# Performance work log

Measured on AMD Instinct MI355X. Metric: run time of the kernel, lower is better.

Reference implementation:

```python
import jax, jax.numpy as jnp
import numpy as np

NEG_SLOPE = 0.01

def lrelu(x):
    return jax.nn.leaky_relu(x, NEG_SLOPE)

def lin(x, w, b):
    # torch Linear: x @ W.T + b, W shape (out, in)
    return x @ w.T + b

def meansum_pool(mask, x_local, *x_global):
    # masked sum + mean over points, concat with global/context vectors
    x_sum = (x_local * mask).sum(axis=1)                 # (b, d)
    x_mean = x_sum / mask.sum(axis=1)                    # (b, d) / (b, 1)
    return jnp.concatenate([x_mean, x_sum, *x_global], axis=1)


def setup_inputs() -> dict:
    key = jax.random.key(0)
    ks = jax.random.split(key, 16)
    B, N, DIN, DC, H, G, NB, DOUT = 16, 8192, 3, 16, 128, 10, 6, 3

    def w(k, shape, fan_in):
        return (jax.random.normal(k, shape, jnp.float32) / np.float32(np.sqrt(fan_in)))

    inp = {
        "x_local": jax.random.normal(ks[0], (B, N, DIN), jnp.float32),
        "context": jax.random.normal(ks[1], (B, DC), jnp.float32),
        "mask": (jax.random.uniform(ks[2], (B, N, 1)) < 0.9).astype(jnp.float32),
        # EPiC_Projection params (effective weight-normed weights)
        "proj_lw": w(ks[3], (H, DIN), DIN), "proj_lb": jnp.zeros((H,), jnp.float32),
        "proj_g0w": w(ks[4], (H, 2 * H + DC), 2 * H + DC), "proj_g0b": jnp.zeros((H,), jnp.float32),
        "proj_g1w": w(ks[5], (H, H), H), "proj_g1b": jnp.zeros((H,), jnp.float32),
        "proj_g2w": w(ks[6], (G, H), H), "proj_g2b": jnp.zeros((G,), jnp.float32),
        # stacked per-block EPiC_layer params
        "g1w": w(ks[7], (NB, H, 2 * H + G + DC), 2 * H + G + DC), "g1b": jnp.zeros((NB, H), jnp.float32),
        "g2w": w(ks[8], (NB, G, H), H), "g2b": jnp.zeros((NB, G), jnp.float32),
        "l1w": w(ks[9], (NB, H, H + G + DC), H + G + DC), "l1b": jnp.zeros((NB, H), jnp.float32),
        "l2w": w(ks[10], (NB, H, H), H), "l2b": jnp.zeros((NB, H), jnp.float32),
        # output head
        "outw": w(ks[11], (DOUT, H), H), "outb": jnp.zeros((DOUT,), jnp.float32),
    }
    return inp


def reference(x_local, context, mask,
              proj_lw, proj_lb, proj_g0w, proj_g0b, proj_g1w, proj_g1b, proj_g2w, proj_g2b,
              g1w, g1b, g2w, g2b, l1w, l1b, l2w, l2b, outw, outb):
    B, N, _ = x_local.shape
    # --- EPiC_Projection ---
    xl = lrelu(lin(x_local, proj_lw, proj_lb))           # (b, n, H)
    xg = meansum_pool(mask, xl, context)                 # (b, 2H + DC)
    xg = lrelu(lin(xg, proj_g0w, proj_g0b))
    xg = lrelu(lin(xg, proj_g1w, proj_g1b))
    xg = lrelu(lin(xg, proj_g2w, proj_g2b))              # (b, G)
    xl = xl * mask
    # --- EPiC layers (no skip: use_skip_connection=False -> +0) ---
    num_blocks = g1w.shape[0]
    for i in range(num_blocks):
        pooled = meansum_pool(mask, xl, xg, context)     # (b, 2H + G + DC)
        h_g = lrelu(lin(pooled, g1w[i], g1b[i]))
        xg = lrelu(lin(h_g, g2w[i], g2b[i]) + xg)        # residual global
        xg_b = jnp.broadcast_to(xg[:, None, :], (B, N, xg.shape[-1]))
        ctx_b = jnp.broadcast_to(context[:, None, :], (B, N, context.shape[-1]))
        cat = jnp.concatenate([xl, xg_b, ctx_b], axis=2)  # (b, n, H + G + DC)
        h_l = lrelu(lin(cat, l1w[i], l1b[i]))
        xl = lrelu(lin(h_l, l2w[i], l2b[i]) + xl) * mask  # residual local, masked
    h = lin(xl, outw, outb)                              # (b, n, 3)
    return h * mask
```

## Files before the change

### kernel.cpp

```cpp
#include <hip/hip_runtime.h>
#include <hip/hip_bf16.h>


typedef __attribute__((ext_vector_type(8))) short short8;
typedef __attribute__((ext_vector_type(4))) float f32x4;

#define B_ 16
#define N_ 8192
#define DC_ 16
#define H_ 128
#define G_ 10
#define NB_ 6
#define NEG_ 0.01f

__device__ __forceinline__ float lrelu(float x) { return x > 0.f ? x : NEG_ * x; }

__device__ __forceinline__ unsigned short f2bf(float x) {
  union { float f; unsigned u; } v; v.f = x;
  return (unsigned short)((v.u + 0x7fffu + ((v.u >> 16) & 1u)) >> 16);
}
__device__ __forceinline__ float bf2f(unsigned short u) {
  union { unsigned u; float f; } v; v.u = ((unsigned)u) << 16; return v.f;
}
__device__ __forceinline__ void split_bf(float x, unsigned short& h, unsigned short& l) {
  h = f2bf(x);
  l = f2bf(x - bf2f(h));
}

__device__ __forceinline__ f32x4 mfma16(short8 a, short8 b, f32x4 c) {
  return __builtin_amdgcn_mfma_f32_16x16x32_bf16(a, b, c, 0, 0, 0);
}

__device__ __forceinline__ void make_frags(f32x4 v0, f32x4 v1, short8& bh, short8& bl) {
  unsigned short h, l;
#pragma unroll
  for (int j = 0; j < 4; ++j) {
    split_bf(v0[j], h, l);
    bh[j] = (short)h; bl[j] = (short)l;
  }
#pragma unroll
  for (int j = 0; j < 4; ++j) {
    split_bf(v1[j], h, l);
    bh[4 + j] = (short)h; bl[4 + j] = (short)l;
  }
}

__device__ __forceinline__ void async_cp16(const void* g, void* l) {
  __builtin_amdgcn_global_load_lds(
      (const __attribute__((address_space(1))) void*)g,
      (__attribute__((address_space(3))) void*)l, 16, 0, 0);
}

__device__ __forceinline__ void agent_store(float* p, float v) {
  __hip_atomic_store(p, v, __ATOMIC_RELAXED, __HIP_MEMORY_SCOPE_AGENT);
}
__device__ __forceinline__ float agent_load(const float* p) {
  return __hip_atomic_load(p, __ATOMIC_RELAXED, __HIP_MEMORY_SCOPE_AGENT);
}

template <int NS>
__device__ void epic_global_tail(
    int b, int tid, const float* __restrict__ pP, float cnt,
    const float* __restrict__ xg_cur, float* __restrict__ xg_next,
    const float* __restrict__ context,
    const float* __restrict__ g1w_n, const float* __restrict__ g1b_n,
    const float* __restrict__ g2w_n, const float* __restrict__ g2b_n,
    const float* __restrict__ l1w_n, const float* __restrict__ l1b_n,
    float* __restrict__ gbias_out, float* shx) {
  {
    const int f = tid & 127, kh = tid >> 7;
    const float* pr = pP + ((size_t)b * NS + kh * (NS / 2)) * 128 + f;
    float s = 0.f;
#pragma unroll 8
    for (int w = 0; w < NS / 2; ++w) s += agent_load(pr + w * 128);
    shx[tid] = s;
  }
  __syncthreads();
  if (tid < 128) {
    float s = shx[tid] + shx[tid + 128];
    shx[384 + tid] = s;
    shx[256 + tid] = s / cnt;
  }
  if (tid < G_) shx[512 + tid] = xg_cur[tid];
  if (tid < DC_) shx[522 + tid] = context[b * DC_ + tid];
  __syncthreads();
  {
    const int f = tid & 127, kh = tid >> 7;
    const float* wr = g1w_n + (size_t)f * 282 + kh * 142;
    const float* vp = shx + 256 + kh * 142;
    const int n2 = kh ? 70 : 71;
    float a = 0.f;
#pragma unroll 8
    for (int j = 0; j < n2; ++j) {
      float2 w2 = *(const float2*)(wr + 2 * j);
      a += w2.x * vp[2 * j] + w2.y * vp[2 * j + 1];
    }
    __syncthreads();
    shx[tid] = a;
  }
  __syncthreads();
  if (tid < 128) shx[544 + tid] = lrelu(shx[tid] + shx[tid + 128] + g1b_n[tid]);
  __syncthreads();
  if (tid < G_) {
    const float* wr = g2w_n + tid * 128;
    float a = g2b_n[tid] + shx[512 + tid];
#pragma unroll 8
    for (int j = 0; j < 32; ++j) {
      float4 w4 = *(const float4*)(wr + 4 * j);
      a += w4.x * shx[544 + 4 * j] + w4.y * shx[544 + 4 * j + 1] +
           w4.z * shx[544 + 4 * j + 2] + w4.w * shx[544 + 4 * j + 3];
    }
    float v = lrelu(a);
    shx[672 + tid] = v;
    xg_next[tid] = v;
  }
  __syncthreads();
  if (tid < 128) {
    const float* wr = l1w_n + tid * 154;
    float a = l1b_n[tid];
#pragma unroll
    for (int j = 0; j < G_; ++j) a += wr[128 + j] * shx[672 + j];
#pragma unroll
    for (int j = 0; j < DC_; ++j) a += wr[138 + j] * shx[522 + j];
    gbias_out[tid] = a;
  }
}

__global__ __launch_bounds__(256) void prep_weights(
    const float* __restrict__ l1w, const float* __restrict__ l2w,
    unsigned short* __restrict__ w1h, unsigned short* __restrict__ w1l,
    unsigned short* __restrict__ w2h, unsigned short* __restrict__ w2l,
    unsigned int* __restrict__ counters) {
  int idx = blockIdx.x * 256 + threadIdx.x;
  const int total = NB_ * H_ * H_;
  if (idx < 112) counters[idx] = 0u;
  if (idx < total) {
    int i = idx / (H_ * H_), rem = idx % (H_ * H_);
    int F = rem / H_, k = rem % H_;
    int mt = F >> 4, r = F & 15, ks = k >> 5, c = k & 31;
    int off = i * 16384 + (mt * 4 + ks) * 512 + ((c >> 3) * 16 + r) * 8 + (c & 7);
    unsigned short h, l;
    split_bf(l1w[(i * H_ + F) * 154 + k], h, l);
    w1h[off] = h; w1l[off] = l;
    split_bf(l2w[(i * H_ + F) * H_ + k], h, l);
    w2h[off] = h; w2l[off] = l;
  }
}

__global__ __launch_bounds__(256, 2) void proj_local_kernel(
    const float* __restrict__ xloc, const float* __restrict__ maskp,
    const float* __restrict__ plw, const float* __restrict__ plb,
    float* __restrict__ xlf, float* __restrict__ pP,
    float* __restrict__ cntp, float* __restrict__ cnt_g,
    unsigned int* __restrict__ counters,
    const float* __restrict__ context,
    const float* __restrict__ g0w, const float* __restrict__ g0b,
    const float* __restrict__ g1pw, const float* __restrict__ g1pb,
    const float* __restrict__ g2pw, const float* __restrict__ g2pb,
    float* __restrict__ xg_g,
    const float* __restrict__ g1w0, const float* __restrict__ g1b0,
    const float* __restrict__ g2w0, const float* __restrict__ g2b0,
    const float* __restrict__ l1w0, const float* __restrict__ l1b0,
    float* __restrict__ gbias_g) {
  __shared__ float wq[H_][4];
  __shared__ float wsum[512];
  __shared__ float cw[4];
  __shared__ float shx[768];
  __shared__ int winflag;
  const int tid = threadIdx.x, bid = blockIdx.x;
  const int wv = tid >> 6, lane = tid & 63;
  const int q = lane >> 4, n16 = lane & 15;
  const int b = bid >> 6;
  if (tid < H_) {
    wq[tid][0] = plw[tid * 3 + 0];
    wq[tid][1] = plw[tid * 3 + 1];
    wq[tid][2] = plw[tid * 3 + 2];
    wq[tid][3] = plb[tid];
  }
  __syncthreads();
  const int t = bid * 4 + wv;
  const int p0 = t * 32;
  const int pa = p0 + n16, pb = p0 + 16 + n16;
  const float xa0 = xloc[pa * 3], xa1 = xloc[pa * 3 + 1], xa2 = xloc[pa * 3 + 2];
  const float xb0 = xloc[pb * 3], xb1 = xloc[pb * 3 + 1], xb2 = xloc[pb * 3 + 2];
  const float m0 = maskp[pa], m1 = maskp[pb];
  float* ga = xlf + (size_t)(2 * t) * 2048;
  float* gb = ga + 2048;
#pragma unroll
  for (int ms = 0; ms < 8; ++ms) {
    f32x4 v0, v1;
#pragma unroll
    for (int r = 0; r < 4; ++r) {
      const int F = ms * 16 + q * 4 + r;
      float4 w4 = *(const float4*)wq[F];
      v0[r] = lrelu(w4.x * xa0 + w4.y * xa1 + w4.z * xa2 + w4.w) * m0;
      v1[r] = lrelu(w4.x * xb0 + w4.y * xb1 + w4.z * xb2 + w4.w) * m1;
    }
    *(f32x4*)(ga + ms * 256 + (q * 16 + n16) * 4) = v0;
    *(f32x4*)(gb + ms * 256 + (q * 16 + n16) * 4) = v1;
    f32x4 s = v0 + v1;
#pragma unroll
    for (int r = 0; r < 4; ++r) {
      float sv = s[r];
      sv += __shfl_xor(sv, 1, 64);
      sv += __shfl_xor(sv, 2, 64);
      sv += __shfl_xor(sv, 4, 64);
      sv += __shfl_xor(sv, 8, 64);
      s[r] = sv;
    }
    if (n16 == 0) *(f32x4*)&wsum[wv * 128 + ms * 16 + q * 4] = s;
  }
  {
    float c = (q == 0) ? (m0 + m1) : 0.f;
    c += __shfl_xor(c, 1, 64);
    c += __shfl_xor(c, 2, 64);
    c += __shfl_xor(c, 4, 64);
    c += __shfl_xor(c, 8, 64);
    if (lane == 0) cw[wv] = c;
  }
  __syncthreads();
  if (tid < 128) {
    agent_store(&pP[(size_t)(2 * bid) * 128 + tid], wsum[tid] + wsum[128 + tid]);
    agent_store(&pP[(size_t)(2 * bid + 1) * 128 + tid], wsum[256 + tid] + wsum[384 + tid]);
  }
  if (tid == 0) agent_store(&cntp[bid], cw[0] + cw[1] + cw[2] + cw[3]);

  __syncthreads();
  if (tid == 0) winflag = (atomicAdd(&counters[b], 1u) == 63u) ? 1 : 0;
  __syncthreads();
  if (!winflag) return;
  if (tid < 64) shx[688 + tid] = agent_load(&cntp[b * 64 + tid]);
  __syncthreads();
  if (tid == 0) {
    float c = 0.f;
#pragma unroll
    for (int w = 0; w < 64; ++w) c += shx[688 + w];
    shx[752] = c;
    cnt_g[b] = c;
  }
  __syncthreads();
  const float cnt = shx[752];
  {
    const int f = tid & 127, kh = tid >> 7;
    const float* pr = pP + ((size_t)b * 128 + kh * 64) * 128 + f;
    float s = 0.f;
#pragma unroll 8
    for (int w = 0; w < 64; ++w) s += agent_load(pr + w * 128);
    shx[tid] = s;
  }
  __syncthreads();
  if (tid < 128) {
    float s = shx[tid] + shx[tid + 128];
    shx[384 + tid] = s;
    shx[256 + tid] = s / cnt;
  }
  if (tid < DC_) shx[512 + tid] = context[b * DC_ + tid];
  __syncthreads();
  {
    const int f = tid & 127, kh = tid >> 7;
    const float* wr = g0w + (size_t)f * 272 + kh * 136;
    const float* vp = shx + 256 + kh * 136;
    float a = 0.f;
#pragma unroll 8
    for (int j = 0; j < 34; ++j) {
      float4 w4 = *(const float4*)(wr + 4 * j);
      a += w4.x * vp[4 * j] + w4.y * vp[4 * j + 1] + w4.z * vp[4 * j + 2] + w4.w * vp[4 * j + 3];
    }
    __syncthreads();
    shx[tid] = a;
  }
  __syncthreads();
  if (tid < 128) shx[544 + tid] = lrelu(shx[tid] + shx[tid + 128] + g0b[tid]);
  __syncthreads();
  {
    const int f = tid & 127, kh = tid >> 7;
    const float* wr = g1pw + (size_t)f * 128 + kh * 64;
    const float* vp = shx + 544 + kh * 64;
    float a = 0.f;
#pragma unroll 8
    for (int j = 0; j < 16; ++j) {
      float4 w4 = *(const float4*)(wr + 4 * j);
      a += w4.x * vp[4 * j] + w4.y * vp[4 * j + 1] + w4.z * vp[4 * j + 2] + w4.w * vp[4 * j + 3];
    }
    __syncthreads();
    shx[tid] = a;
  }
  __syncthreads();
  if (tid < 128) shx[544 + tid] = lrelu(shx[tid] + shx[tid + 128] + g1pb[tid]);
  __syncthreads();
  if (tid < G_) {
    const float* wr = g2pw + tid * 128;
    float a = g2pb[tid];
#pragma unroll 8
    for (int j = 0; j < 32; ++j) {
      float4 w4 = *(const float4*)(wr + 4 * j);
      a += w4.x * shx[544 + 4 * j] + w4.y * shx[544 + 4 * j + 1] +
           w4.z * shx[544 + 4 * j + 2] + w4.w * shx[544 + 4 * j + 3];
    }
    xg_g[(0 * 16 + b) * 16 + tid] = lrelu(a);
  }
  __syncthreads();
  epic_global_tail<128>(b, tid, pP, cnt,
                        xg_g + (0 * 16 + b) * 16, xg_g + (1 * 16 + b) * 16, context,
                        g1w0, g1b0, g2w0, g2b0, l1w0, l1b0,
                        gbias_g + (size_t)(0 * 16 + b) * 128, shx);
}

template <bool LAST>
__global__ __launch_bounds__(256, 1) void epic_local_kernel(
    float* __restrict__ xlf, float* __restrict__ pP,
    const float* __restrict__ cnt_g, unsigned int* __restrict__ counters_blk,
    const float* __restrict__ gbias_in,
    const float* __restrict__ xg_tail_cur, float* __restrict__ xg_tail_next,
    float* __restrict__ gbias_tail_out,
    const float* __restrict__ context,
    const float* __restrict__ g1w_n, const float* __restrict__ g1b_n,
    const float* __restrict__ g2w_n, const float* __restrict__ g2b_n,
    const float* __restrict__ l1w_n, const float* __restrict__ l1b_n,
    const float* __restrict__ l2b,
    const unsigned short* __restrict__ w1h, const unsigned short* __restrict__ w1l,
    const unsigned short* __restrict__ w2h, const unsigned short* __restrict__ w2l,
    const float* __restrict__ maskp,
    const float* __restrict__ outw, const float* __restrict__ outb,
    float* __restrict__ outp) {
  __shared__ unsigned short wbuf[65536];
  __shared__ float tiles[4][576];
  __shared__ float shx[768];
  __shared__ float gbias_s[128];
  __shared__ float l2b_s[128];
  __shared__ float wsum[512];
  __shared__ float outw_s[392];
  __shared__ int winflag;
  const int tid = threadIdx.x, bid = blockIdx.x;
  const int b = bid >> 5;
  const int wv = tid >> 6, lane = tid & 63;
  const int q = lane >> 4, n16 = lane & 15;

  {
    const unsigned short* src = (wv == 0) ? w1h : (wv == 1) ? w1l : (wv == 2) ? w2h : w2l;
    const char* s8 = (const char*)src + lane * 16;
    char* d8 = (char*)&wbuf[wv * 16384];
#pragma unroll
    for (int j = 0; j < 32; ++j) async_cp16(s8 + j * 1024, d8 + j * 1024);
  }
  if (tid < 128) {
    gbias_s[tid] = gbias_in[b * 128 + tid];
    l2b_s[tid] = l2b[tid];
  }
  if (LAST) {
    for (int i = tid; i < 384; i += 256) outw_s[i] = outw[i];
    if (tid < 3) outw_s[384 + tid] = outb[tid];
  }

  const int g0i = bid * 16 + wv * 4;
  short8 xbh[4][4], xbl[4][4];
#pragma unroll
  for (int nt = 0; nt < 4; ++nt) {
    const float* base_nt = xlf + (size_t)(g0i + nt) * 2048;
#pragma unroll
    for (int ks = 0; ks < 4; ++ks) {
      const float* pb = base_nt + (2 * ks + (q >> 1)) * 256 + ((q & 1) * 32 + n16) * 4;
      f32x4 v0 = *(const f32x4*)pb;
      f32x4 v1 = *(const f32x4*)(pb + 64);
      make_frags(v0, v1, xbh[nt][ks], xbl[nt][ks]);
    }
  }
  __syncthreads();

  const unsigned short* w1h_l = wbuf;
  const unsigned short* w1l_l = wbuf + 16384;
  const unsigned short* w2h_l = wbuf + 32768;
  const unsigned short* w2l_l = wbuf + 49152;
  float* T = tiles[wv];
  const int lane16 = lane * 8;

  f32x4 acc2[4][8];
#pragma unroll
  for (int nt = 0; nt < 4; ++nt)
#pragma unroll
    for (int ms = 0; ms < 8; ++ms) acc2[nt][ms] = (f32x4){0.f, 0.f, 0.f, 0.f};

#pragma unroll
  for (int ko = 0; ko < 4; ++ko) {
    short8 a1h[2][4], a1l[2][4];
#pragma unroll
    for (int msl = 0; msl < 2; ++msl)
#pragma unroll
      for (int ks = 0; ks < 4; ++ks) {
        const int off = ((ko * 2 + msl) * 4 + ks) * 512 + lane16;
        a1h[msl][ks] = *(const short8*)(w1h_l + off);
        a1l[msl][ks] = *(const short8*)(w1l_l + off);
      }
    f32x4 acc[4][2];
#pragma unroll
    for (int nt = 0; nt < 4; ++nt)
#pragma unroll
      for (int msl = 0; msl < 2; ++msl) acc[nt][msl] = (f32x4){0.f, 0.f, 0.f, 0.f};
#pragma unroll
    for (int ks = 0; ks < 4; ++ks)
#pragma unroll
      for (int msl = 0; msl < 2; ++msl)
#pragma unroll
        for (int nt = 0; nt < 4; ++nt) {
          acc[nt][msl] = mfma16(a1h[msl][ks], xbh[nt][ks], acc[nt][msl]);
          acc[nt][msl] = mfma16(a1l[msl][ks], xbh[nt][ks], acc[nt][msl]);
          acc[nt][msl] = mfma16(a1h[msl][ks], xbl[nt][ks], acc[nt][msl]);
        }
    short8 b2h[4], b2l[4];
#pragma unroll
    for (int nt = 0; nt < 4; ++nt) {
#pragma unroll
      for (int msl = 0; msl < 2; ++msl) {
        f32x4 gb4 = *(const f32x4*)&gbias_s[(ko * 2 + msl) * 16 + q * 4];
        f32x4 hv;
#pragma unroll
        for (int r = 0; r < 4; ++r) hv[r] = lrelu(acc[nt][msl][r] + gb4[r]);
        *(f32x4*)&T[n16 * 36 + msl * 16 + q * 4] = hv;
      }
      __builtin_amdgcn_wave_barrier();
      {
        f32x4 h0 = *(const f32x4*)&T[n16 * 36 + q * 8];
        f32x4 h1 = *(const f32x4*)&T[n16 * 36 + q * 8 + 4];
        make_frags(h0, h1, b2h[nt], b2l[nt]);
      }
      __builtin_amdgcn_wave_barrier();
    }
    short8 a2h[8], a2l[8];
#pragma unroll
    for (int ms = 0; ms < 8; ++ms) {
      const int off = (ms * 4 + ko) * 512 + lane16;
      a2h[ms] = *(const short8*)(w2h_l + off);
      a2l[ms] = *(const short8*)(w2l_l + off);
    }
#pragma unroll
    for (int ms = 0; ms < 8; ++ms)
#pragma unroll
      for (int nt = 0; nt < 4; ++nt) {
        acc2[nt][ms] = mfma16(a2h[ms], b2h[nt], acc2[nt][ms]);
        acc2[nt][ms] = mfma16(a2l[ms], b2h[nt], acc2[nt][ms]);
        acc2[nt][ms] = mfma16(a2h[ms], b2l[nt], acc2[nt][ms]);
      }
  }

  float mk[4];
#pragma unroll
  for (int nt = 0; nt < 4; ++nt) mk[nt] = maskp[(g0i + nt) * 16 + n16];
  f32x4 vsum[8];
  float po[4][3];
  if (!LAST) {
#pragma unroll
    for (int ms = 0; ms < 8; ++ms) vsum[ms] = (f32x4){0.f, 0.f, 0.f, 0.f};
  } else {
#pragma unroll
    for (int nt = 0; nt < 4; ++nt) po[nt][0] = po[nt][1] = po[nt][2] = 0.f;
  }
#pragma unroll
  for (int nt = 0; nt < 4; ++nt) {
    float* base_nt = xlf + (size_t)(g0i + nt) * 2048;
#pragma unroll
    for (int ms = 0; ms < 8; ++ms) {
      f32x4 lb4 = *(const f32x4*)&l2b_s[ms * 16 + q * 4];
      float* xo = base_nt + ms * 256 + (q * 16 + n16) * 4;
      f32x4 old = *(const f32x4*)xo;
      f32x4 v;
#pragma unroll
      for (int r = 0; r < 4; ++r) v[r] = lrelu(acc2[nt][ms][r] + lb4[r] + old[r]) * mk[nt];
      if (!LAST) {
        *(f32x4*)xo = v;
        vsum[ms] += v;
      } else {
        f32x4 w0 = *(const f32x4*)&outw_s[0 * 128 + ms * 16 + q * 4];
        f32x4 w1 = *(const f32x4*)&outw_s[1 * 128 + ms * 16 + q * 4];
        f32x4 w2 = *(const f32x4*)&outw_s[2 * 128 + ms * 16 + q * 4];
#pragma unroll
        for (int r = 0; r < 4; ++r) {
          po[nt][0] += v[r] * w0[r];
          po[nt][1] += v[r] * w1[r];
          po[nt][2] += v[r] * w2[r];
        }
      }
    }
  }
  if (LAST) {
#pragma unroll
    for (int nt = 0; nt < 4; ++nt)
#pragma unroll
      for (int o = 0; o < 3; ++o) {
        float s = po[nt][o];
        s += __shfl_xor(s, 16, 64);
        s += __shfl_xor(s, 32, 64);
        po[nt][o] = s;
      }
    if (q == 0) {
#pragma unroll
      for (int nt = 0; nt < 4; ++nt) {
        const int p = (g0i + nt) * 16 + n16;
#pragma unroll
        for (int o = 0; o < 3; ++o)
          outp[(size_t)p * 3 + o] = (po[nt][o] + outw_s[384 + o]) * mk[nt];
      }
    }
    return;
  }
#pragma unroll
  for (int ms = 0; ms < 8; ++ms) {
    f32x4 sr;
#pragma unroll
    for (int r = 0; r < 4; ++r) {
      float s = vsum[ms][r];
      s += __shfl_xor(s, 1, 64);
      s += __shfl_xor(s, 2, 64);
      s += __shfl_xor(s, 4, 64);
      s += __shfl_xor(s, 8, 64);
      sr[r] = s;
    }
    if (n16 == 0) *(f32x4*)&wsum[wv * 128 + ms * 16 + q * 4] = sr;
  }
  __syncthreads();
  if (tid < 128)
    agent_store(&pP[(size_t)bid * 128 + tid],
                wsum[tid] + wsum[128 + tid] + wsum[256 + tid] + wsum[384 + tid]);

  __syncthreads();
  if (tid == 0) winflag = (atomicAdd(&counters_blk[b], 1u) == 31u) ? 1 : 0;
  __syncthreads();
  if (!winflag) return;
  epic_global_tail<32>(b, tid, pP, cnt_g[b], xg_tail_cur + b * 16, xg_tail_next + b * 16,
                       context, g1w_n, g1b_n, g2w_n, g2b_n, l1w_n, l1b_n,
                       gbias_tail_out + (size_t)b * 128, shx);
}

extern "C" void kernel_launch(void* const* d_in, const int* in_sizes, int n_in,
                              void* d_out, int out_size, void* d_ws, size_t ws_size,
                              hipStream_t stream) {
  const float* x_local = (const float*)d_in[0];
  const float* context = (const float*)d_in[1];
  const float* mask = (const float*)d_in[2];
  const float* proj_lw = (const float*)d_in[3];
  const float* proj_lb = (const float*)d_in[4];
  const float* proj_g0w = (const float*)d_in[5];
  const float* proj_g0b = (const float*)d_in[6];
  const float* proj_g1w = (const float*)d_in[7];
  const float* proj_g1b = (const float*)d_in[8];
  const float* proj_g2w = (const float*)d_in[9];
  const float* proj_g2b = (const float*)d_in[10];
  const float* g1w = (const float*)d_in[11];
  const float* g1b = (const float*)d_in[12];
  const float* g2w = (const float*)d_in[13];
  const float* g2b = (const float*)d_in[14];
  const float* l1w = (const float*)d_in[15];
  const float* l1b = (const float*)d_in[16];
  const float* l2w = (const float*)d_in[17];
  const float* l2b = (const float*)d_in[18];
  const float* outw = (const float*)d_in[19];
  const float* outb = (const float*)d_in[20];
  float* out = (float*)d_out;

  char* ws = (char*)d_ws;
  float* xlf = (float*)ws;
  float* pP = (float*)(ws + 67108864);
  float* cntp = (float*)(ws + 68157440);
  float* cnt_g = (float*)(ws + 68161536);
  float* xg_g = (float*)(ws + 68161600);
  float* gbias_g = (float*)(ws + 68168768);
  unsigned int* counters = (unsigned int*)(ws + 68217920);
  unsigned short* w1h = (unsigned short*)(ws + 68218368);
  unsigned short* w1l = (unsigned short*)(ws + 68414976);
  unsigned short* w2h = (unsigned short*)(ws + 68611584);
  unsigned short* w2l = (unsigned short*)(ws + 68808192);

  prep_weights<<<384, 256, 0, stream>>>(l1w, l2w, w1h, w1l, w2h, w2l, counters);
  proj_local_kernel<<<1024, 256, 0, stream>>>(
      x_local, mask, proj_lw, proj_lb, xlf, pP, cntp, cnt_g, counters, context,
      proj_g0w, proj_g0b, proj_g1w, proj_g1b, proj_g2w, proj_g2b, xg_g,
      g1w, g1b, g2w, g2b, l1w, l1b, gbias_g);
  for (int i = 0; i < NB_; ++i) {
    const int j = i + 1;
    const float* g1w_n = g1w + (size_t)j * 128 * 282;
    const float* g1b_n = g1b + j * 128;
    const float* g2w_n = g2w + j * 10 * 128;
    const float* g2b_n = g2b + j * 10;
    const float* l1w_n = l1w + (size_t)j * 128 * 154;
    const float* l1b_n = l1b + j * 128;
    const unsigned short* w1h_i = w1h + i * 16384;
    const unsigned short* w1l_i = w1l + i * 16384;
    const unsigned short* w2h_i = w2h + i * 16384;
    const unsigned short* w2l_i = w2l + i * 16384;
    if (i == NB_ - 1) {
      epic_local_kernel<true><<<512, 256, 0, stream>>>(
          xlf, pP, cnt_g, counters + (i + 1) * 16, gbias_g + (size_t)(i * 16) * 128,
          nullptr, nullptr, nullptr, context,
          nullptr, nullptr, nullptr, nullptr, nullptr, nullptr,
          l2b + i * 128, w1h_i, w1l_i, w2h_i, w2l_i, mask, outw, outb, out);
    } else {
      epic_local_kernel<false><<<512, 256, 0, stream>>>(
          xlf, pP, cnt_g, counters + (i + 1) * 16, gbias_g + (size_t)(i * 16) * 128,
          xg_g + (i + 1) * 16 * 16, xg_g + (i + 2) * 16 * 16,
          gbias_g + (size_t)((i + 1) * 16) * 128, context,
          g1w_n, g1b_n, g2w_n, g2b_n, l1w_n, l1b_n,
          l2b + i * 128, w1h_i, w1l_i, w2h_i, w2l_i, mask, outw, outb, out);
    }
  }
}
```

Baseline: 506.3 us.

## Use 512-thread blocks in EPiC local kernel to share weight LDS across more waves

After: 702.7 us. 1.39x slower.

```diff
diff --git a/kernel.cpp b/kernel.cpp
--- a/kernel.cpp
+++ b/kernel.cpp
@@ -23,8 +23,11 @@
   union { unsigned u; float f; } v; v.u = ((unsigned)u) << 16; return v.f;
 }
 __device__ __forceinline__ void split_bf(float x, unsigned short& h, unsigned short& l) {
-  h = f2bf(x);
-  l = f2bf(x - bf2f(h));
+  union { float f; unsigned u; } v; v.f = x;
+  unsigned hu = v.u & 0xffff0000u;
+  h = (unsigned short)(hu >> 16);
+  union { unsigned u; float f; } hv; hv.u = hu;
+  l = f2bf(x - hv.f);
 }
 
 __device__ __forceinline__ f32x4 mfma16(short8 a, short8 b, f32x4 c) {
@@ -67,7 +70,7 @@
     const float* __restrict__ g2w_n, const float* __restrict__ g2b_n,
     const float* __restrict__ l1w_n, const float* __restrict__ l1b_n,
     float* __restrict__ gbias_out, float* shx) {
-  {
+  if (tid < 256) {
     const int f = tid & 127, kh = tid >> 7;
     const float* pr = pP + ((size_t)b * NS + kh * (NS / 2)) * 128 + f;
     float s = 0.f;
@@ -82,9 +85,9 @@
     shx[256 + tid] = s / cnt;
   }
   if (tid < G_) shx[512 + tid] = xg_cur[tid];
-  if (tid < DC_) shx[522 + tid] = context[b * DC_ + tid];
-  __syncthreads();
-  {
+  if (tid >= 32 && tid < 32 + DC_) shx[522 + tid - 32] = context[b * DC_ + tid - 32];
+  __syncthreads();
+  if (tid < 256) {
     const int f = tid & 127, kh = tid >> 7;
     const float* wr = g1w_n + (size_t)f * 282 + kh * 142;
     const float* vp = shx + 256 + kh * 142;
@@ -95,7 +98,6 @@
       float2 w2 = *(const float2*)(wr + 2 * j);
       a += w2.x * vp[2 * j] + w2.y * vp[2 * j + 1];
     }
-    __syncthreads();
     shx[tid] = a;
   }
   __syncthreads();
@@ -307,7 +309,7 @@
 }
 
 template <bool LAST>
-__global__ __launch_bounds__(256, 1) void epic_local_kernel(
+__global__ __launch_bounds__(512, 2) void epic_local_kernel(
     float* __restrict__ xlf, float* __restrict__ pP,
     const float* __restrict__ cnt_g, unsigned int* __restrict__ counters_blk,
     const float* __restrict__ gbias_in,
@@ -324,35 +326,36 @@
     const float* __restrict__ outw, const float* __restrict__ outb,
     float* __restrict__ outp) {
   __shared__ unsigned short wbuf[65536];
-  __shared__ float tiles[4][576];
+  __shared__ float tiles[8][576];
   __shared__ float shx[768];
   __shared__ float gbias_s[128];
   __shared__ float l2b_s[128];
-  __shared__ float wsum[512];
+  __shared__ float wsum[1024];
   __shared__ float outw_s[392];
   __shared__ int winflag;
   const int tid = threadIdx.x, bid = blockIdx.x;
-  const int b = bid >> 5;
+  const int b = bid >> 4;
   const int wv = tid >> 6, lane = tid & 63;
   const int q = lane >> 4, n16 = lane & 15;
 
   {
-    const unsigned short* src = (wv == 0) ? w1h : (wv == 1) ? w1l : (wv == 2) ? w2h : w2l;
-    const char* s8 = (const char*)src + lane * 16;
-    char* d8 = (char*)&wbuf[wv * 16384];
-#pragma unroll
-    for (int j = 0; j < 32; ++j) async_cp16(s8 + j * 1024, d8 + j * 1024);
+    const unsigned short* src =
+        (wv < 2) ? w1h : (wv < 4) ? w1l : (wv < 6) ? w2h : w2l;
+    const char* s8 = (const char*)(src + (wv & 1) * 8192) + lane * 16;
+    char* d8 = (char*)wbuf + wv * 16384;
+#pragma unroll
+    for (int j = 0; j < 16; ++j) async_cp16(s8 + j * 1024, d8 + j * 1024);
   }
   if (tid < 128) {
     gbias_s[tid] = gbias_in[b * 128 + tid];
     l2b_s[tid] = l2b[tid];
   }
   if (LAST) {
-    for (int i = tid; i < 384; i += 256) outw_s[i] = outw[i];
-    if (tid < 3) outw_s[384 + tid] = outb[tid];
-  }
-
-  const int g0i = bid * 16 + wv * 4;
+    if (tid < 384) outw_s[tid] = outw[tid];
+    if (tid >= 384 && tid < 387) outw_s[tid] = outb[tid - 384];
+  }
+
+  const int g0i = bid * 32 + wv * 4;
   short8 xbh[4][4], xbl[4][4];
 #pragma unroll
   for (int nt = 0; nt < 4; ++nt) {
@@ -517,15 +520,18 @@
     if (n16 == 0) *(f32x4*)&wsum[wv * 128 + ms * 16 + q * 4] = sr;
   }
   __syncthreads();
-  if (tid < 128)
-    agent_store(&pP[(size_t)bid * 128 + tid],
-                wsum[tid] + wsum[128 + tid] + wsum[256 + tid] + wsum[384 + tid]);
-
-  __syncthreads();
-  if (tid == 0) winflag = (atomicAdd(&counters_blk[b], 1u) == 31u) ? 1 : 0;
+  if (tid < 128) {
+    float s = 0.f;
+#pragma unroll
+    for (int w = 0; w < 8; ++w) s += wsum[w * 128 + tid];
+    agent_store(&pP[(size_t)bid * 128 + tid], s);
+  }
+
+  __syncthreads();
+  if (tid == 0) winflag = (atomicAdd(&counters_blk[b], 1u) == 15u) ? 1 : 0;
   __syncthreads();
   if (!winflag) return;
-  epic_global_tail<32>(b, tid, pP, cnt_g[b], xg_tail_cur + b * 16, xg_tail_next + b * 16,
+  epic_global_tail<16>(b, tid, pP, cnt_g[b], xg_tail_cur + b * 16, xg_tail_next + b * 16,
                        context, g1w_n, g1b_n, g2w_n, g2b_n, l1w_n, l1b_n,
                        gbias_tail_out + (size_t)b * 128, shx);
 }
@@ -587,13 +593,13 @@
     const unsigned short* w2h_i = w2h + i * 16384;
     const unsigned short* w2l_i = w2l + i * 16384;
     if (i == NB_ - 1) {
-      epic_local_kernel<true><<<512, 256, 0, stream>>>(
+      epic_local_kernel<true><<<256, 512, 0, stream>>>(
           xlf, pP, cnt_g, counters + (i + 1) * 16, gbias_g + (size_t)(i * 16) * 128,
           nullptr, nullptr, nullptr, context,
           nullptr, nullptr, nullptr, nullptr, nullptr, nullptr,
           l2b + i * 128, w1h_i, w1l_i, w2h_i, w2l_i, mask, outw, outb, out);
     } else {
-      epic_local_kernel<false><<<512, 256, 0, stream>>>(
+      epic_local_kernel<false><<<256, 512, 0, stream>>>(
           xlf, pP, cnt_g, counters + (i + 1) * 16, gbias_g + (size_t)(i * 16) * 128,
           xg_g + (i + 1) * 16 * 16, xg_g + (i + 2) * 16 * 16,
           gbias_g + (size_t)((i + 1) * 16) * 128, context,
```
